# Performance work log

Measured on AMD Instinct MI355X. Metric: run time of the kernel, lower is better.

The kernel has to match this reference:

```python
import jax, jax.numpy as jnp
import numpy as np

E = 8           # num_experts
K = 2           # num_experts_per_tok
D = 1024        # hidden_size
F = 2048        # intermediate_dim
B, S = 1, 2048  # batch, seq_len


def setup_inputs() -> dict:
    key = jax.random.key(0)
    k0, k1, k2, k3, k4, k5 = jax.random.split(key, 6)
    hidden_states = jax.random.normal(k0, (B, S, D), dtype=jnp.float32)
    topk_weights = jax.random.uniform(k1, (B * S, K), dtype=jnp.float32)
    topk_ids = jax.random.randint(k2, (B * S, K), 0, E, dtype=jnp.int32)
    scale = 0.02
    wi_0 = jax.random.normal(k3, (E, D, F), dtype=jnp.float32) * scale
    wi_1 = jax.random.normal(k4, (E, D, F), dtype=jnp.float32) * scale
    wo = jax.random.normal(k5, (E, F, D), dtype=jnp.float32) * scale
    return {"hidden_states": hidden_states, "topk_weights": topk_weights,
            "topk_ids": topk_ids, "wi_0": wi_0, "wi_1": wi_1, "wo": wo}


def _gmm(x, w, group_sizes):
    """Grouped matmul: rows of x are sorted by expert; group_sizes[e] rows use w[e].
    Small fixed loop over experts (E=8); rows not owned by expert e are masked out."""
    n_e = w.shape[0]
    expert_of_row = jnp.repeat(jnp.arange(n_e), group_sizes,
                               total_repeat_length=x.shape[0])  # [M]
    out = jnp.zeros((x.shape[0], w.shape[2]), dtype=x.dtype)
    for e in range(n_e):
        out = out + jnp.where((expert_of_row == e)[:, None], x @ w[e], 0.0)
    return out


def _moe_forward(hidden_states, topk_weights, topk_ids, wi_0, wi_1, wo):
    b, s, d = hidden_states.shape
    k = topk_ids.shape[1]
    n_e = wi_0.shape[0]
    x2d = hidden_states.reshape(b * s, d)

    # ---- permute: sort expanded tokens by selected expert (stable) ----
    flat_experts = jnp.ravel(topk_ids)                       # [T*K]
    sort_idx = jnp.argsort(flat_experts, stable=True)        # [T*K]
    sorted_rows = sort_idx // k                              # source token per row
    x_sorted = jnp.take(x2d, sorted_rows, axis=0)            # [T*K, D]
    group_sizes = jnp.bincount(flat_experts, length=n_e)     # [E]

    # ---- grouped GEMMs with SwiGLU (gate * up, then down) ----
    g0 = _gmm(x_sorted, wi_0, group_sizes)                   # [T*K, F]
    g1 = _gmm(x_sorted, wi_1, group_sizes)                   # [T*K, F]
    h = jax.nn.silu(g0) * g1                                 # fused SiLU-gate
    y = _gmm(h, wo, group_sizes)                             # [T*K, D]

    # ---- unpermute and combine with routing weights (fp32 accum) ----
    unsort_idx = jnp.argsort(sort_idx, stable=True)
    y = jnp.take(y, unsort_idx, axis=0).reshape(b * s, k, d)
    out = jnp.einsum('bke,bk->be', y.astype(jnp.float32),
                     topk_weights.astype(jnp.float32))
    return out.reshape(b, s, d)


def reference(hidden_states, topk_weights, topk_ids, wi_0, wi_1, wo):
    return _moe_forward(hidden_states, topk_weights, topk_ids, wi_0, wi_1, wo)
```

## Files before the change

kernel.cpp:

```cpp
#include <hip/hip_runtime.h>
#include <hip/hip_bf16.h>


#define D_DIM 1024
#define F_DIM 2048
#define ROWS 4096
#define MAXTILE 40
#define LDK 72

using f32x4 = __attribute__((ext_vector_type(4))) float;
using s16x8 = __attribute__((ext_vector_type(8))) short;

__device__ __forceinline__ unsigned pack_trunc(float lo, float hi) {
  return (__float_as_uint(lo) >> 16) | (__float_as_uint(hi) & 0xffff0000u);
}
__device__ __forceinline__ unsigned short bf_rn(float f) {
  unsigned u = __float_as_uint(f);
  u += 0x7fffu + ((u >> 16) & 1u);
  return (unsigned short)(u >> 16);
}
__device__ __forceinline__ unsigned pack_rn(float lo, float hi) {
  return (unsigned)bf_rn(lo) | ((unsigned)bf_rn(hi) << 16);
}

typedef const __attribute__((address_space(1))) void* gp_t;
typedef __attribute__((address_space(3))) void* lp_t;
__device__ __forceinline__ void load16(const void* g, void* l) {
  __builtin_amdgcn_global_load_lds((gp_t)g, (lp_t)l, 16, 0, 0);
}

__device__ __forceinline__ void route_body(const int* __restrict__ ids,
                                           int* __restrict__ sorted_flat,
                                           int* __restrict__ unsort,
                                           int* __restrict__ tile_meta,
                                           int* sid, int* cnt, int* off) {
  const int tid = threadIdx.x;
#pragma unroll
  for (int j = 0; j < 2; j++) {
    int idx = tid + j * 512;
    *(int4*)&sid[idx * 4] = *(const int4*)&ids[idx * 4];
  }
  __syncthreads();
  const int w = tid >> 6, lane = tid & 63;
  int c = 0;
  for (int base = 0; base < ROWS; base += 64)
    c += __popcll(__ballot(sid[base + lane] == w));
  if (lane == 0) cnt[w] = c;
  __syncthreads();
  if (tid == 0) {
    int o = 0;
    for (int e = 0; e < 8; e++) { off[e] = o; o += cnt[e]; }
    off[8] = o;
    int nT = 0;
    for (int e = 0; e < 8; e++) {
      for (int r0 = off[e]; r0 < off[e + 1]; r0 += 128) {
        tile_meta[1 + 3 * nT] = r0;
        tile_meta[2 + 3 * nT] = off[e + 1];
        tile_meta[3 + 3 * nT] = e;
        nT++;
      }
    }
    tile_meta[0] = nT;
  }
  __syncthreads();
  int pos = off[w];
  const unsigned long long below = (1ull << lane) - 1ull;
  for (int base = 0; base < ROWS; base += 64) {
    unsigned long long m = __ballot(sid[base + lane] == w);
    if (sid[base + lane] == w) {
      int p = pos + __popcll(m & below);
      sorted_flat[p] = base + lane;
      unsort[base + lane] = p;
    }
    pos += __popcll(m);
  }
}

__global__ __launch_bounds__(512) void route_kernel(const int* __restrict__ ids,
                                                    int* __restrict__ sorted_flat,
                                                    int* __restrict__ unsort,
                                                    int* __restrict__ tile_meta) {
  __shared__ int sid[ROWS];
  __shared__ int cnt[8];
  __shared__ int off[9];
  route_body(ids, sorted_flat, unsort, tile_meta, sid, cnt, off);
}

__global__ void zero_kernel(float4* __restrict__ p, int n4) {
  int i = blockIdx.x * blockDim.x + threadIdx.x;
  if (i < n4) p[i] = float4{0.f, 0.f, 0.f, 0.f};
}

__global__ __launch_bounds__(512, 4) void convT_lds(
    const float* __restrict__ wi0, const float* __restrict__ wi1,
    const float* __restrict__ wo, unsigned short* __restrict__ w0T,
    unsigned short* __restrict__ w1T, unsigned short* __restrict__ woT,
    const int* __restrict__ ids, int* __restrict__ sorted_flat,
    int* __restrict__ unsort, int* __restrict__ tile_meta,
    float4* __restrict__ out4) {
  __shared__ unsigned t[128 * 128];
  const int z = blockIdx.y;
  if (z == 24) {
    if (blockIdx.x != 0) return;
    route_body(ids, sorted_flat, unsort, tile_meta,
               (int*)t, (int*)&t[4096], (int*)&t[4104]);
    return;
  }
  if (z == 25) {
    const int n4 = (ROWS / 2) * D_DIM / 4;
    for (int i = blockIdx.x * 512 + threadIdx.x; i < n4; i += 64 * 512)
      out4[i] = float4{0.f, 0.f, 0.f, 0.f};
    return;
  }
  const int which = z >> 3, e = z & 7;
  const float* S;
  unsigned short* Dp;
  int Kd, Nd, nbits;
  if (which == 0)      { S = wi0; Dp = w0T; Kd = D_DIM; Nd = F_DIM; nbits = 4; }
  else if (which == 1) { S = wi1; Dp = w1T; Kd = D_DIM; Nd = F_DIM; nbits = 4; }
  else                 { S = wo;  Dp = woT; Kd = F_DIM; Nd = D_DIM; nbits = 3; }
  S  += (size_t)e * Kd * Nd;
  Dp += (size_t)e * Kd * Nd;
  const int n0 = (blockIdx.x & ((1 << nbits) - 1)) * 128;
  const int k0 = (blockIdx.x >> nbits) * 256;
  const int tid = threadIdx.x;
  const int nc  = tid & 31;
  const int kpb = tid >> 5;

  float4 v[8][2];
#pragma unroll
  for (int r = 0; r < 8; r++) {
    const int kp = kpb + r * 16;
    const float* p = S + (size_t)(k0 + 2 * kp) * Nd + n0 + nc * 4;
    v[r][0] = *(const float4*)p;
    v[r][1] = *(const float4*)(p + Nd);
  }
  __builtin_amdgcn_sched_barrier(0);

#pragma unroll
  for (int r = 0; r < 8; r++) {
    const int kp = kpb + r * 16;
    const int q = kp >> 2, ql = kp & 3;
    const int col = ((q ^ (nc & 7)) << 2) | ql;
    t[(4 * nc + 0) * 128 + col] = pack_rn(v[r][0].x, v[r][1].x);
    t[(4 * nc + 1) * 128 + col] = pack_rn(v[r][0].y, v[r][1].y);
    t[(4 * nc + 2) * 128 + col] = pack_rn(v[r][0].z, v[r][1].z);
    t[(4 * nc + 3) * 128 + col] = pack_rn(v[r][0].w, v[r][1].w);
  }
  __syncthreads();

  const int c = tid & 31;
#pragma unroll
  for (int s = 0; s < 8; s++) {
    const int n = (tid >> 5) + s * 16;
    const int col = (c ^ ((n >> 2) & 7)) << 2;
    const unsigned* qp = &t[n * 128 + col];
    uint4 o = make_uint4(qp[0], qp[1], qp[2], qp[3]);
    *(uint4*)(Dp + (size_t)(n0 + n) * Kd + k0 + c * 8) = o;
  }
}

__global__ __launch_bounds__(256) void gather_kernel(const float* __restrict__ x,
                                                     const int* __restrict__ sorted_flat,
                                                     unsigned short* __restrict__ xs) {
  const int r = blockIdx.x;
  const int tok = sorted_flat[r] >> 1;
  const float4 v = *(const float4*)(x + (size_t)tok * D_DIM + threadIdx.x * 4);
  *(uint2*)(xs + (size_t)r * D_DIM + threadIdx.x * 4) =
      make_uint2(pack_rn(v.x, v.y), pack_rn(v.z, v.w));
}

__device__ __forceinline__ int sw(int row, int chunk) {
  return row * 64 + ((chunk ^ (row & 7)) << 3);
}

__global__ __launch_bounds__(256, 3) void gemm1_kernel(
    const unsigned short* __restrict__ xs, const unsigned short* __restrict__ w0T,
    const unsigned short* __restrict__ w1T, const int* __restrict__ tile_meta,
    unsigned short* __restrict__ h) {
  __shared__ unsigned short As[128 * 64];
  __shared__ unsigned short B0s[64 * 64];
  __shared__ unsigned short B1s[64 * 64];
  const int tile = blockIdx.x;
  if (tile >= tile_meta[0]) return;
  const int row0 = tile_meta[1 + 3 * tile];
  const int rowEnd = tile_meta[2 + 3 * tile];
  const int e = tile_meta[3 + 3 * tile];
  const int n0 = blockIdx.y * 64;
  const unsigned short* W0 = w0T + ((size_t)e * F_DIM + n0) * D_DIM;
  const unsigned short* W1 = w1T + ((size_t)e * F_DIM + n0) * D_DIM;

  const int tid = threadIdx.x;
  const int lane = tid & 63, wv = tid >> 6;
  const int wm = (wv & 1) * 64, wn = (wv >> 1) * 32;
  const int lm = lane & 15, lq = lane >> 4;
  const int srow = lane >> 3;
  const int skk = ((lane & 7) ^ srow) << 3;

  f32x4 acc0[4][2], acc1[4][2];
#pragma unroll
  for (int i = 0; i < 4; i++)
#pragma unroll
    for (int j = 0; j < 2; j++) { acc0[i][j] = 0.f; acc1[i][j] = 0.f; }

  for (int k0 = 0; k0 < D_DIM; k0 += 64) {
    __syncthreads();
#pragma unroll
    for (int r = 0; r < 4; r++) {
      const int c = r * 4 + wv;
      const int m = c * 8 + srow;
      int mc = row0 + m; if (mc > ROWS - 1) mc = ROWS - 1;
      load16(xs + (size_t)mc * D_DIM + k0 + skk, (char*)As + c * 1024);
    }
#pragma unroll
    for (int r = 0; r < 2; r++) {
      const int c = r * 4 + wv;
      const int m = c * 8 + srow;
      load16(W0 + (size_t)m * D_DIM + k0 + skk, (char*)B0s + c * 1024);
      load16(W1 + (size_t)m * D_DIM + k0 + skk, (char*)B1s + c * 1024);
    }
    __syncthreads();
#pragma unroll
    for (int ks = 0; ks < 64; ks += 32) {
      const int cb = (ks >> 3) + lq;
      s16x8 af[4], b0[2], b1[2];
#pragma unroll
      for (int t = 0; t < 4; t++)
        af[t] = *(const s16x8*)&As[sw(wm + t * 16 + lm, cb)];
#pragma unroll
      for (int t = 0; t < 2; t++) {
        b0[t] = *(const s16x8*)&B0s[sw(wn + t * 16 + lm, cb)];
        b1[t] = *(const s16x8*)&B1s[sw(wn + t * 16 + lm, cb)];
      }
#pragma unroll
      for (int im = 0; im < 4; im++)
#pragma unroll
        for (int in = 0; in < 2; in++) {
          acc0[im][in] = __builtin_amdgcn_mfma_f32_16x16x32_bf16(
              af[im], b0[in], acc0[im][in], 0, 0, 0);
          acc1[im][in] = __builtin_amdgcn_mfma_f32_16x16x32_bf16(
              af[im], b1[in], acc1[im][in], 0, 0, 0);
        }
    }
  }
#pragma unroll
  for (int im = 0; im < 4; im++) {
    int gmB = row0 + wm + im * 16 + lq * 4;
#pragma unroll
    for (int in = 0; in < 2; in++) {
      int gn = n0 + wn + in * 16 + lm;
#pragma unroll
      for (int r = 0; r < 4; r++) {
        int gm = gmB + r;
        if (gm < rowEnd) {
          float g = acc0[im][in][r];
          float s = g / (1.f + __expf(-g));
          h[(size_t)gm * F_DIM + gn] = bf_rn(s * acc1[im][in][r]);
        }
      }
    }
  }
}

__global__ __launch_bounds__(256, 4) void gemm2_kernel(
    const unsigned short* __restrict__ h, const unsigned short* __restrict__ woT,
    const float* __restrict__ tw, const int* __restrict__ sorted_flat,
    const int* __restrict__ tile_meta, float* __restrict__ out) {
  __shared__ unsigned short As[128 * 64];
  __shared__ unsigned short Bs[64 * 64];
  __shared__ int sTok[128];
  __shared__ float sWgt[128];
  const int tile = blockIdx.x;
  if (tile >= tile_meta[0]) return;
  const int row0 = tile_meta[1 + 3 * tile];
  const int rowEnd = tile_meta[2 + 3 * tile];
  const int e = tile_meta[3 + 3 * tile];
  const int n0 = blockIdx.y * 64;
  const unsigned short* W = woT + ((size_t)e * D_DIM + n0) * F_DIM;

  const int tid = threadIdx.x;
  if (tid < 128) {
    int r = row0 + tid; if (r > ROWS - 1) r = ROWS - 1;
    int fl = sorted_flat[r];
    sTok[tid] = fl >> 1;
    sWgt[tid] = tw[fl];
  }
  const int lane = tid & 63, wv = tid >> 6;
  const int wm = (wv & 1) * 64, wn = (wv >> 1) * 32;
  const int lm = lane & 15, lq = lane >> 4;
  const int srow = lane >> 3;
  const int skk = ((lane & 7) ^ srow) << 3;

  f32x4 acc[4][2];
#pragma unroll
  for (int i = 0; i < 4; i++)
#pragma unroll
    for (int j = 0; j < 2; j++) acc[i][j] = 0.f;

  for (int k0 = 0; k0 < F_DIM; k0 += 64) {
    __syncthreads();
#pragma unroll
    for (int r = 0; r < 4; r++) {
      const int c = r * 4 + wv;
      const int m = c * 8 + srow;
      int mc = row0 + m; if (mc > ROWS - 1) mc = ROWS - 1;
      load16(h + (size_t)mc * F_DIM + k0 + skk, (char*)As + c * 1024);
    }
#pragma unroll
    for (int r = 0; r < 2; r++) {
      const int c = r * 4 + wv;
      const int m = c * 8 + srow;
      load16(W + (size_t)m * F_DIM + k0 + skk, (char*)Bs + c * 1024);
    }
    __syncthreads();
#pragma unroll
    for (int ks = 0; ks < 64; ks += 32) {
      const int cb = (ks >> 3) + lq;
      s16x8 af[4], bf[2];
#pragma unroll
      for (int t = 0; t < 4; t++)
        af[t] = *(const s16x8*)&As[sw(wm + t * 16 + lm, cb)];
#pragma unroll
      for (int t = 0; t < 2; t++)
        bf[t] = *(const s16x8*)&Bs[sw(wn + t * 16 + lm, cb)];
#pragma unroll
      for (int im = 0; im < 4; im++)
#pragma unroll
        for (int in = 0; in < 2; in++)
          acc[im][in] = __builtin_amdgcn_mfma_f32_16x16x32_bf16(
              af[im], bf[in], acc[im][in], 0, 0, 0);
    }
  }
#pragma unroll
  for (int im = 0; im < 4; im++) {
    int lrB = wm + im * 16 + lq * 4;
#pragma unroll
    for (int in = 0; in < 2; in++) {
      int gn = n0 + wn + in * 16 + lm;
#pragma unroll
      for (int r = 0; r < 4; r++) {
        int lr = lrB + r;
        int gm = row0 + lr;
        if (gm < rowEnd)
          atomicAdd(out + (size_t)sTok[lr] * D_DIM + gn,
                    sWgt[lr] * acc[im][in][r]);
      }
    }
  }
}

__device__ __forceinline__ void stage_bt(const float* __restrict__ Wt, int ldw,
                                         unsigned short* Bs, int tid) {
#pragma unroll
  for (int it = 0; it < 4; it++) {
    const int kp = (tid & 7) + it * 8;
    const int nq = tid >> 3;
    const float* p = Wt + (size_t)(2 * kp) * ldw + nq * 4;
    const float4 va = *(const float4*)p;
    const float4 vb = *(const float4*)(p + ldw);
    unsigned short* b = Bs + (nq * 4) * LDK + 2 * kp;
    *(unsigned*)(b)           = pack_trunc(va.x, vb.x);
    *(unsigned*)(b + LDK)     = pack_trunc(va.y, vb.y);
    *(unsigned*)(b + 2 * LDK) = pack_trunc(va.z, vb.z);
    *(unsigned*)(b + 3 * LDK) = pack_trunc(va.w, vb.w);
  }
}

__global__ __launch_bounds__(256, 2) void gemm1_fb(
    const float* __restrict__ x, const float* __restrict__ wi0,
    const float* __restrict__ wi1, const int* __restrict__ sorted_flat,
    const int* __restrict__ tile_meta, unsigned short* __restrict__ h) {
  __shared__ unsigned short As[128 * LDK];
  __shared__ unsigned short B0s[128 * LDK];
  __shared__ unsigned short B1s[128 * LDK];
  __shared__ int tok[128];
  const int tile = blockIdx.x;
  if (tile >= tile_meta[0]) return;
  const int row0 = tile_meta[1 + 3 * tile];
  const int rowEnd = tile_meta[2 + 3 * tile];
  const int e = tile_meta[3 + 3 * tile];
  const int n0 = blockIdx.y * 128;
  const float* W0 = wi0 + (size_t)e * D_DIM * F_DIM;
  const float* W1 = wi1 + (size_t)e * D_DIM * F_DIM;
  const int tid = threadIdx.x;
  if (tid < 128) {
    int r = row0 + tid; if (r > ROWS - 1) r = ROWS - 1;
    tok[tid] = sorted_flat[r] >> 1;
  }
  f32x4 acc0[4][4], acc1[4][4];
#pragma unroll
  for (int i = 0; i < 4; i++)
#pragma unroll
    for (int j = 0; j < 4; j++) { acc0[i][j] = 0.f; acc1[i][j] = 0.f; }
  const int lane = tid & 63, wv = tid >> 6;
  const int wm = (wv & 1) * 64, wn = (wv >> 1) * 64;
  const int lm = lane & 15, lq = lane >> 4;
  for (int k0 = 0; k0 < D_DIM; k0 += 64) {
    __syncthreads();
#pragma unroll
    for (int i = 0; i < 8; i++) {
      int idx = tid + i * 256;
      int m = idx >> 4, kq = idx & 15;
      float4 v = *(const float4*)(x + (size_t)tok[m] * D_DIM + k0 + kq * 4);
      *(uint2*)&As[m * LDK + kq * 4] =
          make_uint2(pack_trunc(v.x, v.y), pack_trunc(v.z, v.w));
    }
    stage_bt(W0 + (size_t)k0 * F_DIM + n0, F_DIM, B0s, tid);
    stage_bt(W1 + (size_t)k0 * F_DIM + n0, F_DIM, B1s, tid);
    __syncthreads();
#pragma unroll
    for (int ks = 0; ks < 64; ks += 32) {
      s16x8 af[4], b0[4], b1[4];
#pragma unroll
      for (int t = 0; t < 4; t++) {
        af[t] = *(const s16x8*)&As[(wm + t * 16 + lm) * LDK + ks + lq * 8];
        b0[t] = *(const s16x8*)&B0s[(wn + t * 16 + lm) * LDK + ks + lq * 8];
        b1[t] = *(const s16x8*)&B1s[(wn + t * 16 + lm) * LDK + ks + lq * 8];
      }
#pragma unroll
      for (int im = 0; im < 4; im++)
#pragma unroll
        for (int in = 0; in < 4; in++) {
          acc0[im][in] = __builtin_amdgcn_mfma_f32_16x16x32_bf16(
              af[im], b0[in], acc0[im][in], 0, 0, 0);
          acc1[im][in] = __builtin_amdgcn_mfma_f32_16x16x32_bf16(
              af[im], b1[in], acc1[im][in], 0, 0, 0);
        }
    }
  }
#pragma unroll
  for (int im = 0; im < 4; im++) {
    int gmB = row0 + wm + im * 16 + lq * 4;
#pragma unroll
    for (int in = 0; in < 4; in++) {
      int gn = n0 + wn + in * 16 + lm;
#pragma unroll
      for (int r = 0; r < 4; r++) {
        int gm = gmB + r;
        if (gm < rowEnd) {
          float g = acc0[im][in][r];
          float s = g / (1.f + __expf(-g));
          h[(size_t)gm * F_DIM + gn] = bf_rn(s * acc1[im][in][r]);
        }
      }
    }
  }
}

__global__ __launch_bounds__(256, 3) void gemm2_fb(
    const unsigned short* __restrict__ h, const float* __restrict__ wo,
    const float* __restrict__ tw, const int* __restrict__ sorted_flat,
    const int* __restrict__ tile_meta, float* __restrict__ out) {
  __shared__ unsigned short As[128 * LDK];
  __shared__ unsigned short Bs[128 * LDK];
  __shared__ int sTok[128];
  __shared__ float sWgt[128];
  const int tile = blockIdx.x;
  if (tile >= tile_meta[0]) return;
  const int row0 = tile_meta[1 + 3 * tile];
  const int rowEnd = tile_meta[2 + 3 * tile];
  const int e = tile_meta[3 + 3 * tile];
  const int n0 = blockIdx.y * 128;
  const float* W = wo + (size_t)e * F_DIM * D_DIM;
  const int tid = threadIdx.x;
  if (tid < 128) {
    int r = row0 + tid; if (r > ROWS - 1) r = ROWS - 1;
    int fl = sorted_flat[r];
    sTok[tid] = fl >> 1;
    sWgt[tid] = tw[fl];
  }
  f32x4 acc[4][4];
#pragma unroll
  for (int i = 0; i < 4; i++)
#pragma unroll
    for (int j = 0; j < 4; j++) acc[i][j] = 0.f;
  const int lane = tid & 63, wv = tid >> 6;
  const int wm = (wv & 1) * 64, wn = (wv >> 1) * 64;
  const int lm = lane & 15, lq = lane >> 4;
  for (int k0 = 0; k0 < F_DIM; k0 += 64) {
    __syncthreads();
#pragma unroll
    for (int i = 0; i < 8; i++) {
      int idx = tid + i * 256;
      int m = idx >> 4, kq = idx & 15;
      int gm = row0 + m; if (gm > ROWS - 1) gm = ROWS - 1;
      *(uint2*)&As[m * LDK + kq * 4] =
          *(const uint2*)(h + (size_t)gm * F_DIM + k0 + kq * 4);
    }
    stage_bt(W + (size_t)k0 * D_DIM + n0, D_DIM, Bs, tid);
    __syncthreads();
#pragma unroll
    for (int ks = 0; ks < 64; ks += 32) {
      s16x8 af[4], bf[4];
#pragma unroll
      for (int t = 0; t < 4; t++) {
        af[t] = *(const s16x8*)&As[(wm + t * 16 + lm) * LDK + ks + lq * 8];
        bf[t] = *(const s16x8*)&Bs[(wn + t * 16 + lm) * LDK + ks + lq * 8];
      }
#pragma unroll
      for (int im = 0; im < 4; im++)
#pragma unroll
        for (int in = 0; in < 4; in++)
          acc[im][in] = __builtin_amdgcn_mfma_f32_16x16x32_bf16(
              af[im], bf[in], acc[im][in], 0, 0, 0);
    }
  }
#pragma unroll
  for (int im = 0; im < 4; im++) {
    int lrB = wm + im * 16 + lq * 4;
#pragma unroll
    for (int in = 0; in < 4; in++) {
      int gn = n0 + wn + in * 16 + lm;
#pragma unroll
      for (int r = 0; r < 4; r++) {
        int lr = lrB + r;
        int gm = row0 + lr;
        if (gm < rowEnd)
          atomicAdd(out + (size_t)sTok[lr] * D_DIM + gn, sWgt[lr] * acc[im][in][r]);
      }
    }
  }
}

extern "C" void kernel_launch(void* const* d_in, const int* in_sizes, int n_in,
                              void* d_out, int out_size, void* d_ws, size_t ws_size,
                              hipStream_t stream) {
  const float* x   = (const float*)d_in[0];
  const float* tw  = (const float*)d_in[1];
  const int*   ids = (const int*)d_in[2];
  const float* wi0 = (const float*)d_in[3];
  const float* wi1 = (const float*)d_in[4];
  const float* wo  = (const float*)d_in[5];
  float* out = (float*)d_out;

  int* tile_meta = (int*)d_ws;
  int* sorted_flat = tile_meta + 256;
  int* unsort = sorted_flat + ROWS;

  const size_t MB = 1024 * 1024;
  const size_t XS_OFF = 64 * 1024;
  const size_t H_OFF  = XS_OFF + 8 * MB;
  const size_t W0_OFF = H_OFF + 16 * MB;
  const size_t W1_OFF = W0_OFF + 32 * MB;
  const size_t WO_OFF = W1_OFF + 32 * MB;
  const size_t NEED   = WO_OFF + 32 * MB;

  if (ws_size >= NEED) {
    unsigned short* xs  = (unsigned short*)((char*)d_ws + XS_OFF);
    unsigned short* h   = (unsigned short*)((char*)d_ws + H_OFF);
    unsigned short* w0T = (unsigned short*)((char*)d_ws + W0_OFF);
    unsigned short* w1T = (unsigned short*)((char*)d_ws + W1_OFF);
    unsigned short* woT = (unsigned short*)((char*)d_ws + WO_OFF);

    convT_lds<<<dim3(64, 26), 512, 0, stream>>>(wi0, wi1, wo, w0T, w1T, woT,
                                                ids, sorted_flat, unsort,
                                                tile_meta, (float4*)out);
    gather_kernel<<<ROWS, 256, 0, stream>>>(x, sorted_flat, xs);
    gemm1_kernel<<<dim3(MAXTILE, F_DIM / 64), 256, 0, stream>>>(xs, w0T, w1T,
                                                                tile_meta, h);
    gemm2_kernel<<<dim3(MAXTILE, D_DIM / 64), 256, 0, stream>>>(h, woT, tw,
                                                                sorted_flat,
                                                                tile_meta, out);
  } else {
    unsigned short* h = (unsigned short*)((char*)d_ws + XS_OFF);
    route_kernel<<<1, 512, 0, stream>>>(ids, sorted_flat, unsort, tile_meta);
    zero_kernel<<<(ROWS / 2 * D_DIM / 4 + 255) / 256, 256, 0, stream>>>(
        (float4*)out, ROWS / 2 * D_DIM / 4);
    gemm1_fb<<<dim3(MAXTILE, F_DIM / 128), 256, 0, stream>>>(x, wi0, wi1,
                                                             sorted_flat,
                                                             tile_meta, h);
    gemm2_fb<<<dim3(MAXTILE, D_DIM / 128), 256, 0, stream>>>(h, wo, tw,
                                                             sorted_flat,
                                                             tile_meta, out);
  }
}
```

Measured before the change: 315.4 us.

## Move wo transpose-convert into gemm1 launch as extra blocks to overlap

Splits the weight transpose/bf16 conversion kernel so only wi_0/wi_1 are converted up front, while the wo conversion runs as extra blocks appended to the gemm1 grid. This lets the memory-bound wo conversion overlap with the compute-bound first grouped GEMM instead of sitting on the critical path before it. The wo blocks use 256 threads with a smaller tile layout and share the gemm1 LDS buffer. This adds block-scheduling contention and may reduce gemm1 occupancy or delay its tiles.

```diff
diff --git a/kernel.cpp b/kernel.cpp
--- a/kernel.cpp
+++ b/kernel.cpp
@@ -91,38 +91,31 @@
   if (i < n4) p[i] = float4{0.f, 0.f, 0.f, 0.f};
 }
 
-__global__ __launch_bounds__(512, 4) void convT_lds(
+__global__ __launch_bounds__(512, 4) void convT_wi(
     const float* __restrict__ wi0, const float* __restrict__ wi1,
-    const float* __restrict__ wo, unsigned short* __restrict__ w0T,
-    unsigned short* __restrict__ w1T, unsigned short* __restrict__ woT,
+    unsigned short* __restrict__ w0T, unsigned short* __restrict__ w1T,
     const int* __restrict__ ids, int* __restrict__ sorted_flat,
     int* __restrict__ unsort, int* __restrict__ tile_meta,
     float4* __restrict__ out4) {
   __shared__ unsigned t[128 * 128];
   const int z = blockIdx.y;
-  if (z == 24) {
+  if (z == 16) {
     if (blockIdx.x != 0) return;
     route_body(ids, sorted_flat, unsort, tile_meta,
                (int*)t, (int*)&t[4096], (int*)&t[4104]);
     return;
   }
-  if (z == 25) {
+  if (z == 17) {
     const int n4 = (ROWS / 2) * D_DIM / 4;
     for (int i = blockIdx.x * 512 + threadIdx.x; i < n4; i += 64 * 512)
       out4[i] = float4{0.f, 0.f, 0.f, 0.f};
     return;
   }
   const int which = z >> 3, e = z & 7;
-  const float* S;
-  unsigned short* Dp;
-  int Kd, Nd, nbits;
-  if (which == 0)      { S = wi0; Dp = w0T; Kd = D_DIM; Nd = F_DIM; nbits = 4; }
-  else if (which == 1) { S = wi1; Dp = w1T; Kd = D_DIM; Nd = F_DIM; nbits = 4; }
-  else                 { S = wo;  Dp = woT; Kd = F_DIM; Nd = D_DIM; nbits = 3; }
-  S  += (size_t)e * Kd * Nd;
-  Dp += (size_t)e * Kd * Nd;
-  const int n0 = (blockIdx.x & ((1 << nbits) - 1)) * 128;
-  const int k0 = (blockIdx.x >> nbits) * 256;
+  const float* S = (which == 0 ? wi0 : wi1) + (size_t)e * D_DIM * F_DIM;
+  unsigned short* Dp = (which == 0 ? w0T : w1T) + (size_t)e * D_DIM * F_DIM;
+  const int n0 = (blockIdx.x & 15) * 128;
+  const int k0 = (blockIdx.x >> 4) * 256;
   const int tid = threadIdx.x;
   const int nc  = tid & 31;
   const int kpb = tid >> 5;
@@ -131,9 +124,9 @@
 #pragma unroll
   for (int r = 0; r < 8; r++) {
     const int kp = kpb + r * 16;
-    const float* p = S + (size_t)(k0 + 2 * kp) * Nd + n0 + nc * 4;
+    const float* p = S + (size_t)(k0 + 2 * kp) * F_DIM + n0 + nc * 4;
     v[r][0] = *(const float4*)p;
-    v[r][1] = *(const float4*)(p + Nd);
+    v[r][1] = *(const float4*)(p + F_DIM);
   }
   __builtin_amdgcn_sched_barrier(0);
 
@@ -156,7 +149,51 @@
     const int col = (c ^ ((n >> 2) & 7)) << 2;
     const unsigned* qp = &t[n * 128 + col];
     uint4 o = make_uint4(qp[0], qp[1], qp[2], qp[3]);
-    *(uint4*)(Dp + (size_t)(n0 + n) * Kd + k0 + c * 8) = o;
+    *(uint4*)(Dp + (size_t)(n0 + n) * D_DIM + k0 + c * 8) = o;
+  }
+}
+
+__device__ __forceinline__ void convT_wo_body(const float* __restrict__ wo,
+                                              unsigned short* __restrict__ woT,
+                                              int id, unsigned* t) {
+  const int e = id >> 7, rem = id & 127;
+  const int k0 = (rem >> 3) * 128;
+  const int n0 = (rem & 7) * 128;
+  const float* S = wo + (size_t)e * F_DIM * D_DIM;
+  unsigned short* Dp = woT + (size_t)e * F_DIM * D_DIM;
+  const int tid = threadIdx.x;
+  const int nc = tid & 31, kpb = tid >> 5;
+
+  float4 v[8][2];
+#pragma unroll
+  for (int r = 0; r < 8; r++) {
+    const int kp = kpb + r * 8;
+    const float* p = S + (size_t)(k0 + 2 * kp) * D_DIM + n0 + nc * 4;
+    v[r][0] = *(const float4*)p;
+    v[r][1] = *(const float4*)(p + D_DIM);
+  }
+  __builtin_amdgcn_sched_barrier(0);
+
+#pragma unroll
+  for (int r = 0; r < 8; r++) {
+    const int kp = kpb + r * 8;
+    const int ch = kp >> 2, ql = kp & 3;
+    const int col = ((ch ^ (nc & 7)) << 2) | ql;
+    t[(4 * nc + 0) * 64 + col] = pack_rn(v[r][0].x, v[r][1].x);
+    t[(4 * nc + 1) * 64 + col] = pack_rn(v[r][0].y, v[r][1].y);
+    t[(4 * nc + 2) * 64 + col] = pack_rn(v[r][0].z, v[r][1].z);
+    t[(4 * nc + 3) * 64 + col] = pack_rn(v[r][0].w, v[r][1].w);
+  }
+  __syncthreads();
+
+  const int c = tid & 15;
+#pragma unroll
+  for (int s = 0; s < 8; s++) {
+    const int n = (tid >> 4) + s * 16;
+    const int col = (c ^ ((n >> 2) & 7)) << 2;
+    const unsigned* qp = &t[n * 64 + col];
+    uint4 o = make_uint4(qp[0], qp[1], qp[2], qp[3]);
+    *(uint4*)(Dp + (size_t)(n0 + n) * F_DIM + k0 + c * 8) = o;
   }
 }
 
@@ -177,10 +214,17 @@
 __global__ __launch_bounds__(256, 3) void gemm1_kernel(
     const unsigned short* __restrict__ xs, const unsigned short* __restrict__ w0T,
     const unsigned short* __restrict__ w1T, const int* __restrict__ tile_meta,
-    unsigned short* __restrict__ h) {
-  __shared__ unsigned short As[128 * 64];
-  __shared__ unsigned short B0s[64 * 64];
-  __shared__ unsigned short B1s[64 * 64];
+    unsigned short* __restrict__ h, const float* __restrict__ wo,
+    unsigned short* __restrict__ woT) {
+  __shared__ unsigned short SH[16384];
+  if (blockIdx.x >= MAXTILE) {
+    convT_wo_body(wo, woT, (int)(blockIdx.x - MAXTILE) + 32 * (int)blockIdx.y,
+                  (unsigned*)SH);
+    return;
+  }
+  unsigned short* As  = SH;
+  unsigned short* B0s = SH + 8192;
+  unsigned short* B1s = SH + 12288;
   const int tile = blockIdx.x;
   if (tile >= tile_meta[0]) return;
   const int row0 = tile_meta[1 + 3 * tile];
@@ -552,24 +596,24 @@
     unsigned short* w1T = (unsigned short*)((char*)d_ws + W1_OFF);
     unsigned short* woT = (unsigned short*)((char*)d_ws + WO_OFF);
 
-    convT_lds<<<dim3(64, 26), 512, 0, stream>>>(wi0, wi1, wo, w0T, w1T, woT,
-                                                ids, sorted_flat, unsort,
-                                                tile_meta, (float4*)out);
+    convT_wi<<<dim3(64, 18), 512, 0, stream>>>(wi0, wi1, w0T, w1T,
+                                               ids, sorted_flat, unsort,
+                                               tile_meta, (float4*)out);
     gather_kernel<<<ROWS, 256, 0, stream>>>(x, sorted_flat, xs);
-    gemm1_kernel<<<dim3(MAXTILE, F_DIM / 64), 256, 0, stream>>>(xs, w0T, w1T,
-                                                                tile_meta, h);
+    gemm1_kernel<<<dim3(MAXTILE + 32, F_DIM / 64), 256, 0, stream>>>(
+        xs, w0T, w1T, tile_meta, h, wo, woT);
     gemm2_kernel<<<dim3(MAXTILE, D_DIM / 64), 256, 0, stream>>>(h, woT, tw,
                                                                 sorted_flat,
                                                                 tile_meta, out);
   } else {
-    unsigned short* h = (unsigned short*)((char*)d_ws + XS_OFF);
+    unsigned short* hfb = (unsigned short*)((char*)d_ws + XS_OFF);
     route_kernel<<<1, 512, 0, stream>>>(ids, sorted_flat, unsort, tile_meta);
     zero_kernel<<<(ROWS / 2 * D_DIM / 4 + 255) / 256, 256, 0, stream>>>(
         (float4*)out, ROWS / 2 * D_DIM / 4);
     gemm1_fb<<<dim3(MAXTILE, F_DIM / 128), 256, 0, stream>>>(x, wi0, wi1,
                                                              sorted_flat,
-                                                             tile_meta, h);
-    gemm2_fb<<<dim3(MAXTILE, D_DIM / 128), 256, 0, stream>>>(h, wo, tw,
+                                                             tile_meta, hfb);
+    gemm2_fb<<<dim3(MAXTILE, D_DIM / 128), 256, 0, stream>>>(hfb, wo, tw,
                                                              sorted_flat,
                                                              tile_meta, out);
   }
```

Result: no change. 313.7 us (-0.5%).
